# Optimization experiments

Measured on AMD Instinct MI355X. Metric: run time of the kernel, lower is better.

## Reference

```python
import jax, jax.numpy as jnp
import numpy as np

DEPTH = 64
N_HEAD = 8
FF = 128
EPS = 1e-5


def layer_norm(x, g, b):
    mu = jnp.mean(x, axis=-1, keepdims=True)
    var = jnp.mean((x - mu) ** 2, axis=-1, keepdims=True)
    return (x - mu) * jax.lax.rsqrt(var + EPS) * g + b


def setup_inputs() -> dict:
    key = jax.random.key(0)
    ks = jax.random.split(key, 16)
    B, S, d, h = 4, 512, DEPTH, N_HEAD
    s = 1.0 / np.sqrt(d)
    return {
        "seq": jax.random.normal(ks[0], (B, S, d), jnp.float32),
        "pos_enc": jax.random.normal(ks[1], (B, S, S, d), jnp.float32),
        "Wq": jax.random.normal(ks[2], (d, d * h), jnp.float32) * s,
        "Wk": jax.random.normal(ks[3], (d, d * h), jnp.float32) * s,
        "Wv": jax.random.normal(ks[4], (d, d * h), jnp.float32) * s,
        "Wo": jax.random.normal(ks[5], (d * h, d), jnp.float32) / np.sqrt(d * h),
        "Wp": jax.random.normal(ks[6], (d, h), jnp.float32) * s,
        "bp": jnp.zeros((h,), jnp.float32),
        "W1": jax.random.normal(ks[7], (d, FF), jnp.float32) * s,
        "b1": jnp.zeros((FF,), jnp.float32),
        "W2": jax.random.normal(ks[8], (FF, d), jnp.float32) / np.sqrt(FF),
        "b2": jnp.zeros((d,), jnp.float32),
        "g_att": jnp.ones((d,), jnp.float32),
        "b_att": jnp.zeros((d,), jnp.float32),
        "g_ff": jnp.ones((d,), jnp.float32),
        "b_ff": jnp.zeros((d,), jnp.float32),
    }


def reference(seq, pos_enc, Wq, Wk, Wv, Wo, Wp, bp, W1, b1, W2, b2, g_att, b_att, g_ff, b_ff):
    B, S, d = seq.shape
    h = N_HEAD
    # QKV: [B,S,h,d] -> [B,h,S,d]; head_dim == depth in this module
    q = (seq @ Wq).reshape(B, S, h, d).transpose(0, 2, 1, 3)
    k = (seq @ Wk).reshape(B, S, h, d).transpose(0, 2, 1, 3)
    v = (seq @ Wv).reshape(B, S, h, d).transpose(0, 2, 1, 3)
    a = jnp.einsum('bhid,bhjd->bhij', q, k) / jnp.sqrt(jnp.asarray(d, seq.dtype))
    # additive learned positional bias: [B,S,S,d] @ [d,h] -> [B,S,S,h] -> [B,h,S,S]
    p = jnp.einsum('bijd,dh->bhij', pos_enc, Wp) + bp[None, :, None, None]
    a = jax.nn.softmax(a + p, axis=-1)
    heads = jnp.einsum('bhij,bhjd->bhid', a, v)  # [B,h,S,d]
    o = heads.transpose(0, 2, 1, 3).reshape(B, S, h * d) @ Wo
    x = layer_norm(seq + o, g_att, b_att)
    y = jax.nn.relu(x @ W1 + b1) @ W2 + b2
    return layer_norm(x + y, g_ff, b_ff)
```

## Files before the change

### kernel.cpp

```cpp
#include <hip/hip_runtime.h>
#include <hip/hip_bf16.h>

#define DEPTH 64
#define NH 8
#define SEQL 512
#define BATCH 4
#define FFDIM 128
#define PROJ (DEPTH*NH)
#define LOG2E 1.44269504088896340736f

typedef __hip_bfloat16 bf16;
typedef __attribute__((ext_vector_type(8))) short short8;
typedef __attribute__((ext_vector_type(4))) float floatx4;

__device__ __forceinline__ short f2bs(float f) {
    __hip_bfloat16 h = __float2bfloat16(f);
    return *reinterpret_cast<short*>(&h);
}
__device__ __forceinline__ float bs2f(short s) {
    __hip_bfloat16 h = *reinterpret_cast<__hip_bfloat16*>(&s);
    return __bfloat162float(h);
}

__global__ __launch_bounds__(256) void qkv_kernel(
    const float* __restrict__ seq, const float* __restrict__ Wq,
    const float* __restrict__ Wk, const float* __restrict__ Wv,
    bf16* __restrict__ q, bf16* __restrict__ k, bf16* __restrict__ vT)
{
    __shared__ __align__(16) short sS[64][72];
    __shared__ __align__(16) short sW[128][72];
    __shared__ __align__(16) short sT[128][72];
    int t = threadIdx.x;
    int lane = t & 63, w = t >> 6;
    const float* W; int vflag = 0;
    bf16* out;
    if (blockIdx.z == 0)      { W = Wq; out = q; }
    else if (blockIdx.z == 1) { W = Wk; out = k; }
    else                      { W = Wv; out = vT; vflag = 1; }
    int m0 = blockIdx.x * 64;
    int n0 = blockIdx.y * 128;

    for (int idx = t; idx < 4096; idx += 256) {
        int r = idx >> 6, kk = idx & 63;
        sS[r][kk] = f2bs(seq[(long)(m0 + r)*64 + kk]);
    }
    for (int idx = t; idx < 8192; idx += 256) {
        int kk = idx >> 7, n = idx & 127;
        sW[n][kk] = f2bs(W[kk*512 + n0 + n]);
    }
    __syncthreads();

    int ln = lane & 15, g4 = lane >> 4;
    int mt = w;
    floatx4 acc[2][4];
    #pragma unroll
    for (int nh = 0; nh < 2; nh++)
        #pragma unroll
        for (int nt = 0; nt < 4; nt++) acc[nh][nt] = (floatx4){0.f,0.f,0.f,0.f};
    #pragma unroll
    for (int ks = 0; ks < 2; ks++) {
        short8 af = *(const short8*)&sS[mt*16 + ln][ks*32 + g4*8];
        #pragma unroll
        for (int nh = 0; nh < 2; nh++)
            #pragma unroll
            for (int nt = 0; nt < 4; nt++) {
                short8 bfv = *(const short8*)&sW[nh*64 + nt*16 + ln][ks*32 + g4*8];
                acc[nh][nt] = __builtin_amdgcn_mfma_f32_16x16x32_bf16(af, bfv, acc[nh][nt], 0, 0, 0);
            }
    }

    if (!vflag) {
        #pragma unroll
        for (int nh = 0; nh < 2; nh++)
            #pragma unroll
            for (int nt = 0; nt < 4; nt++)
                #pragma unroll
                for (int r = 0; r < 4; r++) {
                    int grow = m0 + mt*16 + g4*4 + r;
                    int col  = n0 + nh*64 + nt*16 + ln;
                    int b = grow >> 9, s = grow & 511;
                    int h = col >> 6, d = col & 63;
                    out[(((long)(b*8 + h)*512) + s)*64 + d] = __float2bfloat16(acc[nh][nt][r]);
                }
    } else {
        #pragma unroll
        for (int nh = 0; nh < 2; nh++)
            #pragma unroll
            for (int nt = 0; nt < 4; nt++)
                #pragma unroll
                for (int r = 0; r < 4; r++)
                    sT[nh*64 + nt*16 + ln][mt*16 + g4*4 + r] = f2bs(acc[nh][nt][r]);
        __syncthreads();
        int b = m0 >> 9, s0 = m0 & 511;
        for (int idx = t; idx < 1024; idx += 256) {
            int lc = idx >> 3, c8 = idx & 7;
            *(uint4*)(out + ((long)(b*512 + n0 + lc))*512 + s0 + c8*8) =
                *(const uint4*)&sT[lc][c8*8];
        }
    }
}

__global__ __launch_bounds__(256, 8) void pbias_kernel(
    const float* __restrict__ pos, const float* __restrict__ Wp,
    const float* __restrict__ bp, bf16* __restrict__ p)
{
    __shared__ __align__(16) float sW2[4][132];
    __shared__ float sb[8];
    int t = threadIdx.x;
    for (int i = t; i < 512; i += 256) {
        int sub = i >> 7, rest = i & 127;
        int lk = rest >> 3, h = rest & 7;
        int kk = ((lk >> 2) << 4) + sub*4 + (lk & 3);
        sW2[sub][lk*8 + h] = Wp[kk*8 + h];
    }
    if (t < 8) sb[t] = bp[t];
    __syncthreads();

    int sub = t & 3;
    int lr = t >> 2;
    long rowA = (long)blockIdx.x*128 + lr;
    long rowB = rowA + 64;

    const float4* srcA = (const float4*)(pos + rowA*64);
    const float4* srcB = (const float4*)(pos + rowB*64);
    float4 chA[4], chB[4];
    #pragma unroll
    for (int i = 0; i < 4; i++) chA[i] = srcA[i*4 + sub];
    #pragma unroll
    for (int i = 0; i < 4; i++) chB[i] = srcB[i*4 + sub];

    float accA[8], accB[8];
    #pragma unroll
    for (int h = 0; h < 8; h++) { accA[h] = 0.f; accB[h] = 0.f; }
    #pragma unroll
    for (int i = 0; i < 4; i++) {
        #pragma unroll
        for (int e = 0; e < 4; e++) {
            int lk = i*4 + e;
            const float4* wr = (const float4*)&sW2[sub][lk*8];
            float4 wa = wr[0], wb = wr[1];
            float xA = ((const float*)&chA[i])[e];
            float xB = ((const float*)&chB[i])[e];
            accA[0] += xA*wa.x; accA[1] += xA*wa.y; accA[2] += xA*wa.z; accA[3] += xA*wa.w;
            accA[4] += xA*wb.x; accA[5] += xA*wb.y; accA[6] += xA*wb.z; accA[7] += xA*wb.w;
            accB[0] += xB*wa.x; accB[1] += xB*wa.y; accB[2] += xB*wa.z; accB[3] += xB*wa.w;
            accB[4] += xB*wb.x; accB[5] += xB*wb.y; accB[6] += xB*wb.z; accB[7] += xB*wb.w;
        }
    }
    #pragma unroll
    for (int h = 0; h < 8; h++) {
        accA[h] += __shfl_xor(accA[h], 1, 64);
        accA[h] += __shfl_xor(accA[h], 2, 64);
        accB[h] += __shfl_xor(accB[h], 1, 64);
        accB[h] += __shfl_xor(accB[h], 2, 64);
    }
    if (sub == 0) {
        short8 vA, vB;
        #pragma unroll
        for (int h = 0; h < 8; h++) {
            vA[h] = f2bs(accA[h] + sb[h]);
            vB[h] = f2bs(accB[h] + sb[h]);
        }
        *(short8*)(p + rowA*8) = vA;
        *(short8*)(p + rowB*8) = vB;
    }
}

__global__ __launch_bounds__(256) void attn_kernel(
    const bf16* __restrict__ q, const bf16* __restrict__ k,
    const bf16* __restrict__ vT, const bf16* __restrict__ p,
    bf16* __restrict__ heads)
{
    __shared__ __align__(16) short sQ[64*72];
    __shared__ __align__(16) short sK[64*72];
    __shared__ __align__(16) short sV[64*72];
    __shared__ __align__(16) short sP[4][16*72];

    int t = threadIdx.x;
    int lane = t & 63, w = t >> 6;
    int bid = blockIdx.x;
    int it = bid & 7;
    int bh = bid >> 3;
    int i0 = it*64;
    int b = bh >> 3, h = bh & 7;

    const bf16* qb = q + ((long)bh*SEQL + i0)*DEPTH;
    const bf16* kb = k + (long)bh*SEQL*DEPTH;
    const bf16* vb = vT + (long)bh*DEPTH*SEQL;
    const bf16* pb = p + (((long)b*512 + i0)*512)*8 + h;

    for (int c = t; c < 512; c += 256) {
        int r = c >> 3, c8 = c & 7;
        *(uint4*)((char*)sQ + r*144 + c8*16) = *(const uint4*)(qb + r*64 + c8*8);
    }

    int ln = lane & 15, g4 = lane >> 4;
    float lsum[4];
    floatx4 oacc[4];
    #pragma unroll
    for (int r = 0; r < 4; r++) lsum[r] = 0.f;
    #pragma unroll
    for (int ds = 0; ds < 4; ds++) oacc[ds] = (floatx4){0.f,0.f,0.f,0.f};

    unsigned short pf[16];
    #pragma unroll
    for (int js = 0; js < 4; js++)
        #pragma unroll
        for (int r = 0; r < 4; r++)
            pf[js*4 + r] = *(const unsigned short*)&pb[((long)(w*16 + g4*4 + r)*512 + js*16 + ln)*8];

    for (int jt = 0; jt < 8; jt++) {
        __syncthreads();
        int j0 = jt*64;
        for (int c = t; c < 512; c += 256) {
            int r = c >> 3, c8 = c & 7;
            *(uint4*)((char*)sK + r*144 + c8*16) = *(const uint4*)(kb + (long)(j0 + r)*64 + c8*8);
        }
        for (int c = t; c < 512; c += 256) {
            int r = c >> 3, c8 = c & 7;
            *(uint4*)((char*)sV + r*144 + c8*16) = *(const uint4*)(vb + (long)r*512 + j0 + c8*8);
        }
        __syncthreads();

        unsigned short cur[16];
        #pragma unroll
        for (int e = 0; e < 16; e++) cur[e] = pf[e];
        if (jt < 7) {
            int jn = (jt + 1)*64;
            #pragma unroll
            for (int js = 0; js < 4; js++)
                #pragma unroll
                for (int r = 0; r < 4; r++)
                    pf[js*4 + r] = *(const unsigned short*)&pb[((long)(w*16 + g4*4 + r)*512 + jn + js*16 + ln)*8];
        }

        floatx4 sacc[4];
        #pragma unroll
        for (int js = 0; js < 4; js++) sacc[js] = (floatx4){0.f,0.f,0.f,0.f};
        #pragma unroll
        for (int kk = 0; kk < 2; kk++) {
            short8 aq = *(const short8*)((const char*)sQ + (w*16 + ln)*144 + kk*64 + g4*16);
            #pragma unroll
            for (int js = 0; js < 4; js++) {
                short8 bk = *(const short8*)((const char*)sK + (js*16 + ln)*144 + kk*64 + g4*16);
                sacc[js] = __builtin_amdgcn_mfma_f32_16x16x32_bf16(aq, bk, sacc[js], 0, 0, 0);
            }
        }
        #pragma unroll
        for (int js = 0; js < 4; js++)
            #pragma unroll
            for (int r = 0; r < 4; r++) {
                float pv = bs2f((short)cur[js*4 + r]);
                float e = exp2f((sacc[js][r]*0.125f + pv)*LOG2E);
                lsum[r] += e;
                sP[w][(g4*4 + r)*72 + js*16 + ln] = f2bs(e);
            }
        #pragma unroll
        for (int kk = 0; kk < 2; kk++) {
            short8 ap = *(const short8*)((const char*)sP[w] + ln*144 + kk*64 + g4*16);
            #pragma unroll
            for (int ds = 0; ds < 4; ds++) {
                short8 bv = *(const short8*)((const char*)sV + (ds*16 + ln)*144 + kk*64 + g4*16);
                oacc[ds] = __builtin_amdgcn_mfma_f32_16x16x32_bf16(ap, bv, oacc[ds], 0, 0, 0);
            }
        }
    }

    #pragma unroll
    for (int r = 0; r < 4; r++)
        #pragma unroll
        for (int m = 1; m < 16; m <<= 1) lsum[r] += __shfl_xor(lsum[r], m, 64);

    #pragma unroll
    for (int ds = 0; ds < 4; ds++)
        #pragma unroll
        for (int r = 0; r < 4; r++) {
            float val = oacc[ds][r] / lsum[r];
            int gi = i0 + w*16 + g4*4 + r;
            int col = h*64 + ds*16 + ln;
            heads[((long)b*SEQL + gi)*PROJ + col] = __float2bfloat16(val);
        }
}

__global__ __launch_bounds__(256) void tail_kernel(
    const bf16* __restrict__ heads, const float* __restrict__ Wo,
    const float* __restrict__ seq, const float* __restrict__ g_att,
    const float* __restrict__ b_att, const float* __restrict__ W1,
    const float* __restrict__ b1, const float* __restrict__ W2,
    const float* __restrict__ b2, const float* __restrict__ g_ff,
    const float* __restrict__ b_ff, float* __restrict__ out)
{
    __shared__ __align__(16) short sH[8][520];
    __shared__ float sX[8][68];
    __shared__ float sHid[8][132];
    int t = threadIdx.x;
    int w = t >> 6, lane = t & 63;
    long g0 = (long)blockIdx.x*8;

    for (int idx = t; idx < 512; idx += 256) {
        int r = idx >> 6, c8 = idx & 63;
        *(uint4*)((char*)&sH[r][0] + c8*16) = *(const uint4*)(heads + (g0 + r)*PROJ + c8*8);
    }
    __syncthreads();

    int r0 = w*2, r1 = w*2 + 1;
    float acc0 = 0.f, acc1 = 0.f;
    #pragma unroll 4
    for (int kk8 = 0; kk8 < 64; kk8++) {
        short8 a0 = *(const short8*)&sH[r0][kk8*8];
        short8 a1 = *(const short8*)&sH[r1][kk8*8];
        #pragma unroll
        for (int e = 0; e < 8; e++) {
            float wv = Wo[(kk8*8 + e)*DEPTH + lane];
            acc0 += bs2f(a0[e])*wv;
            acc1 += bs2f(a1[e])*wv;
        }
    }
    float ga = g_att[lane], ba = b_att[lane];
    float xn[2];
    #pragma unroll
    for (int rr = 0; rr < 2; rr++) {
        long row = g0 + w*2 + rr;
        float x0 = (rr ? acc1 : acc0) + seq[row*DEPTH + lane];
        float s1 = x0, s2 = x0*x0;
        #pragma unroll
        for (int m = 1; m < 64; m <<= 1) { s1 += __shfl_xor(s1, m, 64); s2 += __shfl_xor(s2, m, 64); }
        float mu = s1*(1.f/64.f);
        float var = s2*(1.f/64.f) - mu*mu;
        float rstd = rsqrtf(var + 1e-5f);
        xn[rr] = (x0 - mu)*rstd*ga + ba;
        sX[w*2 + rr][lane] = xn[rr];
    }

    float b1a = b1[lane], b1b = b1[lane + 64];
    float h00 = b1a, h01 = b1b, h10 = b1a, h11 = b1b;
    #pragma unroll 4
    for (int kk = 0; kk < DEPTH; kk++) {
        float w0 = W1[kk*FFDIM + lane];
        float w1 = W1[kk*FFDIM + 64 + lane];
        float x0v = sX[r0][kk], x1v = sX[r1][kk];
        h00 += x0v*w0; h01 += x0v*w1;
        h10 += x1v*w0; h11 += x1v*w1;
    }
    sHid[r0][lane] = fmaxf(h00, 0.f); sHid[r0][lane + 64] = fmaxf(h01, 0.f);
    sHid[r1][lane] = fmaxf(h10, 0.f); sHid[r1][lane + 64] = fmaxf(h11, 0.f);

    float bb = b2[lane];
    float acc20 = bb, acc21 = bb;
    #pragma unroll 4
    for (int kk = 0; kk < FFDIM; kk++) {
        float wv = W2[kk*DEPTH + lane];
        acc20 += sHid[r0][kk]*wv;
        acc21 += sHid[r1][kk]*wv;
    }
    float gf = g_ff[lane], bf = b_ff[lane];
    #pragma unroll
    for (int rr = 0; rr < 2; rr++) {
        long row = g0 + w*2 + rr;
        float z = xn[rr] + (rr ? acc21 : acc20);
        float t1 = z, t2 = z*z;
        #pragma unroll
        for (int m = 1; m < 64; m <<= 1) { t1 += __shfl_xor(t1, m, 64); t2 += __shfl_xor(t2, m, 64); }
        float mu2 = t1*(1.f/64.f);
        float var2 = t2*(1.f/64.f) - mu2*mu2;
        float rstd2 = rsqrtf(var2 + 1e-5f);
        out[row*DEPTH + lane] = (z - mu2)*rstd2*gf + bf;
    }
}

extern "C" void kernel_launch(void* const* d_in, const int* in_sizes, int n_in,
                              void* d_out, int out_size, void* d_ws, size_t ws_size,
                              hipStream_t stream) {
    const float* seq   = (const float*)d_in[0];
    const float* pos   = (const float*)d_in[1];
    const float* Wq    = (const float*)d_in[2];
    const float* Wk    = (const float*)d_in[3];
    const float* Wv    = (const float*)d_in[4];
    const float* Wo    = (const float*)d_in[5];
    const float* Wp    = (const float*)d_in[6];
    const float* bp    = (const float*)d_in[7];
    const float* W1    = (const float*)d_in[8];
    const float* b1    = (const float*)d_in[9];
    const float* W2    = (const float*)d_in[10];
    const float* b2    = (const float*)d_in[11];
    const float* g_att = (const float*)d_in[12];
    const float* b_att = (const float*)d_in[13];
    const float* g_ff  = (const float*)d_in[14];
    const float* b_ff  = (const float*)d_in[15];
    float* outp = (float*)d_out;

    bf16* qb  = (bf16*)d_ws;
    bf16* kb  = qb + 1048576;
    bf16* vTb = kb + 1048576;
    bf16* pb  = vTb + 1048576;
    bf16* hb  = pb + 8388608;

    qkv_kernel  <<<dim3(32, 4, 3), 256, 0, stream>>>(seq, Wq, Wk, Wv, qb, kb, vTb);
    pbias_kernel<<<8192,           256, 0, stream>>>(pos, Wp, bp, pb);
    attn_kernel <<<256,            256, 0, stream>>>(qb, kb, vTb, pb, hb);
    tail_kernel <<<256,            256, 0, stream>>>(hb, Wo, seq, g_att, b_att,
                                                     W1, b1, W2, b2, g_ff, b_ff, outp);
}
```

Measured before the change: 113.6 us.

## Restructure positional-bias kernel into grid-stride loop with register weights and prefetch

The positional-bias projection kernel now keeps the Wp weights in registers instead of shared memory, which removes the shared-memory staging and the barrier. Each thread handles 8 rows in a strided loop with software prefetch of the next row. Eight threads split each 64-wide row, and each thread's two float4 loads are 32 floats apart. The grid is halved and launch bounds are relaxed. This targets the memory-bound streaming of the 134MB pos_enc tensor. It costs more registers, an extra shuffle stage, and possibly lower occupancy.

```diff
diff --git a/kernel.cpp b/kernel.cpp
--- a/kernel.cpp
+++ b/kernel.cpp
@@ -100,69 +100,68 @@
     }
 }
 
-__global__ __launch_bounds__(256, 8) void pbias_kernel(
+__global__ __launch_bounds__(256, 4) void pbias_kernel(
     const float* __restrict__ pos, const float* __restrict__ Wp,
     const float* __restrict__ bp, bf16* __restrict__ p)
 {
-    __shared__ __align__(16) float sW2[4][132];
-    __shared__ float sb[8];
     int t = threadIdx.x;
-    for (int i = t; i < 512; i += 256) {
-        int sub = i >> 7, rest = i & 127;
-        int lk = rest >> 3, h = rest & 7;
-        int kk = ((lk >> 2) << 4) + sub*4 + (lk & 3);
-        sW2[sub][lk*8 + h] = Wp[kk*8 + h];
-    }
-    if (t < 8) sb[t] = bp[t];
-    __syncthreads();
-
-    int sub = t & 3;
-    int lr = t >> 2;
-    long rowA = (long)blockIdx.x*128 + lr;
-    long rowB = rowA + 64;
-
-    const float4* srcA = (const float4*)(pos + rowA*64);
-    const float4* srcB = (const float4*)(pos + rowB*64);
-    float4 chA[4], chB[4];
-    #pragma unroll
-    for (int i = 0; i < 4; i++) chA[i] = srcA[i*4 + sub];
-    #pragma unroll
-    for (int i = 0; i < 4; i++) chB[i] = srcB[i*4 + sub];
-
-    float accA[8], accB[8];
-    #pragma unroll
-    for (int h = 0; h < 8; h++) { accA[h] = 0.f; accB[h] = 0.f; }
-    #pragma unroll
-    for (int i = 0; i < 4; i++) {
+    int sub = t & 7;
+    int lr  = t >> 3;
+
+    float4 wA[4], wB[4], wC[4], wD[4];
+    #pragma unroll
+    for (int e = 0; e < 4; e++) {
+        int k0 = sub*4 + e, k1 = 32 + sub*4 + e;
+        wA[e] = *(const float4*)&Wp[k0*8];
+        wB[e] = *(const float4*)&Wp[k0*8 + 4];
+        wC[e] = *(const float4*)&Wp[k1*8];
+        wD[e] = *(const float4*)&Wp[k1*8 + 4];
+    }
+    float bias[8];
+    #pragma unroll
+    for (int h = 0; h < 8; h++) bias[h] = bp[h];
+
+    const long rstride = (long)4096*32;
+    long row = (long)blockIdx.x*32 + lr;
+
+    float4 c0 = *(const float4*)(pos + row*64 + sub*4);
+    float4 c1 = *(const float4*)(pos + row*64 + 32 + sub*4);
+
+    #pragma unroll
+    for (int it = 0; it < 8; it++) {
+        long nrow = row + rstride;
+        float4 n0, n1;
+        if (it < 7) {
+            n0 = *(const float4*)(pos + nrow*64 + sub*4);
+            n1 = *(const float4*)(pos + nrow*64 + 32 + sub*4);
+        }
+
+        float acc[8];
+        #pragma unroll
+        for (int h = 0; h < 8; h++) acc[h] = 0.f;
         #pragma unroll
         for (int e = 0; e < 4; e++) {
-            int lk = i*4 + e;
-            const float4* wr = (const float4*)&sW2[sub][lk*8];
-            float4 wa = wr[0], wb = wr[1];
-            float xA = ((const float*)&chA[i])[e];
-            float xB = ((const float*)&chB[i])[e];
-            accA[0] += xA*wa.x; accA[1] += xA*wa.y; accA[2] += xA*wa.z; accA[3] += xA*wa.w;
-            accA[4] += xA*wb.x; accA[5] += xA*wb.y; accA[6] += xA*wb.z; accA[7] += xA*wb.w;
-            accB[0] += xB*wa.x; accB[1] += xB*wa.y; accB[2] += xB*wa.z; accB[3] += xB*wa.w;
-            accB[4] += xB*wb.x; accB[5] += xB*wb.y; accB[6] += xB*wb.z; accB[7] += xB*wb.w;
-        }
-    }
-    #pragma unroll
-    for (int h = 0; h < 8; h++) {
-        accA[h] += __shfl_xor(accA[h], 1, 64);
-        accA[h] += __shfl_xor(accA[h], 2, 64);
-        accB[h] += __shfl_xor(accB[h], 1, 64);
-        accB[h] += __shfl_xor(accB[h], 2, 64);
-    }
-    if (sub == 0) {
-        short8 vA, vB;
+            float x0 = ((const float*)&c0)[e];
+            float x1 = ((const float*)&c1)[e];
+            acc[0] += x0*wA[e].x; acc[1] += x0*wA[e].y; acc[2] += x0*wA[e].z; acc[3] += x0*wA[e].w;
+            acc[4] += x0*wB[e].x; acc[5] += x0*wB[e].y; acc[6] += x0*wB[e].z; acc[7] += x0*wB[e].w;
+            acc[0] += x1*wC[e].x; acc[1] += x1*wC[e].y; acc[2] += x1*wC[e].z; acc[3] += x1*wC[e].w;
+            acc[4] += x1*wD[e].x; acc[5] += x1*wD[e].y; acc[6] += x1*wD[e].z; acc[7] += x1*wD[e].w;
+        }
         #pragma unroll
         for (int h = 0; h < 8; h++) {
-            vA[h] = f2bs(accA[h] + sb[h]);
-            vB[h] = f2bs(accB[h] + sb[h]);
-        }
-        *(short8*)(p + rowA*8) = vA;
-        *(short8*)(p + rowB*8) = vB;
+            acc[h] += __shfl_xor(acc[h], 1, 64);
+            acc[h] += __shfl_xor(acc[h], 2, 64);
+            acc[h] += __shfl_xor(acc[h], 4, 64);
+        }
+        if (sub == 0) {
+            short8 v;
+            #pragma unroll
+            for (int h = 0; h < 8; h++) v[h] = f2bs(acc[h] + bias[h]);
+            *(short8*)(p + row*8) = v;
+        }
+        c0 = n0; c1 = n1;
+        row = nrow;
     }
 }
 
@@ -396,7 +395,7 @@
     bf16* hb  = pb + 8388608;
 
     qkv_kernel  <<<dim3(32, 4, 3), 256, 0, stream>>>(seq, Wq, Wk, Wv, qb, kb, vTb);
-    pbias_kernel<<<8192,           256, 0, stream>>>(pos, Wp, bp, pb);
+    pbias_kernel<<<4096,           256, 0, stream>>>(pos, Wp, bp, pb);
     attn_kernel <<<256,            256, 0, stream>>>(qb, kb, vTb, pb, hb);
     tail_kernel <<<256,            256, 0, stream>>>(hb, Wo, seq, g_att, b_att,
                                                      W1, b1, W2, b2, g_ff, b_ff, outp);
```

Result: slower. 132.2 us (+16.3%).
